# Kernel tuning notes

Hardware: AMD Instinct MI355X
Metric: run time of the kernel (lower is better)

Reference implementation:

```python
import jax, jax.numpy as jnp
import numpy as np

B, N, C, S, H, E = 4, 50000, 128, 64, 8, 800000
DH = C // H
BETA = 1.0      # frontier_beta
EPS = 1e-5      # LayerNorm eps


def setup_inputs() -> dict:
    key = jax.random.key(0)
    ks = jax.random.split(key, 12)
    sc = 1.0 / np.sqrt(C)
    x = jax.random.normal(ks[0], (B, N, C), jnp.float32)
    adj_indices = jax.random.randint(ks[1], (2, E), 0, N)
    adj_values = jax.random.uniform(ks[2], (E,), jnp.float32)
    return {
        "x": x,
        "adj_values": adj_values,
        "ln_g": jnp.ones((C,), jnp.float32),
        "ln_b": jnp.zeros((C,), jnp.float32),
        "slice_w": jax.random.normal(ks[3], (S, C), jnp.float32) * sc,
        "slice_b": jnp.zeros((S,), jnp.float32),
        "front_w": jax.random.normal(ks[4], (S, C), jnp.float32) * sc,
        "front_b": jnp.zeros((S,), jnp.float32),
        "in_w": jax.random.normal(ks[5], (3 * C, C), jnp.float32) * sc,
        "in_b": jnp.zeros((3 * C,), jnp.float32),
        "out_w": jax.random.normal(ks[6], (C, C), jnp.float32) * sc,
        "out_b": jnp.zeros((C,), jnp.float32),
        "adj_indices": adj_indices,
    }


def _layernorm(x, g, b):
    m = x.mean(-1, keepdims=True)
    v = ((x - m) ** 2).mean(-1, keepdims=True)
    return (x - m) / jnp.sqrt(v + EPS) * g + b


def reference(x, adj_values, ln_g, ln_b, slice_w, slice_b, front_w, front_b,
              in_w, in_b, out_w, out_b, adj_indices):
    h = _layernorm(x, ln_g, ln_b)                                   # (B,N,C)
    rows, cols = adj_indices[0], adj_indices[1]
    # SpMM: y[b, r] += val * h[b, c] over edges (coalesce() sums duplicates,
    # identical to segment_sum over duplicate (r,c) pairs)
    gathered = h[:, cols, :] * adj_values[None, :, None]            # (B,E,C)
    h_local = jax.vmap(
        lambda g: jax.ops.segment_sum(g, rows, num_segments=N))(gathered)
    h_frontier = h - h_local
    logits = (h @ slice_w.T + slice_b
              + BETA * (h_frontier @ front_w.T + front_b))          # (B,N,S)
    weights = jax.nn.softmax(logits, axis=-1)
    wsum = jnp.maximum(weights.sum(axis=1), 1e-8)[:, :, None]       # (B,S,1)
    slices = jnp.einsum('bns,bnc->bsc', weights, h) / wsum          # (B,S,C)
    # MultiheadAttention (batch_first, self-attention) on slice tokens
    qkv = slices @ in_w.T + in_b                                    # (B,S,3C)
    q, k, v = jnp.split(qkv, 3, axis=-1)
    split_heads = lambda t: t.reshape(B, S, H, DH).transpose(0, 2, 1, 3)
    q, k, v = split_heads(q), split_heads(k), split_heads(v)        # (B,H,S,DH)
    attn = jax.nn.softmax(
        jnp.einsum('bhqd,bhkd->bhqk', q, k) / np.sqrt(DH), axis=-1)
    o = jnp.einsum('bhqk,bhkd->bhqd', attn, v)
    o = o.transpose(0, 2, 1, 3).reshape(B, S, C)
    slices_out = o @ out_w.T + out_b                                # (B,S,C)
    out = jnp.einsum('bns,bsc->bnc', weights, slices_out)           # (B,N,C)
    return out, weights
```

## Files before the change

kernel.cpp:

```cpp
#include <hip/hip_runtime.h>
#include <math.h>

#define NB 4
#define NN 50000
#define NC 128
#define NS 64
#define NH 8
#define NE 800000
#define NDH 16
#define RTOT (NB*NN)
#define NCHUNK 128
#define NSB 196
#define LN_EPS 1e-5f

typedef __bf16 bf16;
typedef bf16 bf16x2 __attribute__((ext_vector_type(2)));
typedef bf16 bf16x4 __attribute__((ext_vector_type(4)));
typedef bf16 bf16x8 __attribute__((ext_vector_type(8)));
typedef float f32x4 __attribute__((ext_vector_type(4)));

__device__ __forceinline__ float wsum64(float v){
  #pragma unroll
  for (int off = 32; off; off >>= 1) v += __shfl_xor(v, off, 64);
  return v;
}
__device__ __forceinline__ float wmax64(float v){
  #pragma unroll
  for (int off = 32; off; off >>= 1) v = fmaxf(v, __shfl_xor(v, off, 64));
  return v;
}

__global__ void k_hist(const int* __restrict__ rows, int* __restrict__ counts){
  int e = blockIdx.x * 256 + threadIdx.x;
  if (e < NE) atomicAdd(&counts[rows[e]], 1);
}

__global__ void k_scan1(const int* __restrict__ counts,
    int* __restrict__ locpre, int* __restrict__ bsum){
  __shared__ int sh[256];
  int t = threadIdx.x;
  int gid = blockIdx.x * 256 + t;
  int v = (gid < NN) ? counts[gid] : 0;
  sh[t] = v;
  __syncthreads();
  #pragma unroll
  for (int off = 1; off < 256; off <<= 1){
    int u = (t >= off) ? sh[t - off] : 0;
    __syncthreads();
    sh[t] += u;
    __syncthreads();
  }
  if (gid < NN) locpre[gid] = sh[t] - v;
  if (t == 255) bsum[blockIdx.x] = sh[255];
}

__global__ void k_scan2(const int* __restrict__ bsum,
    int* __restrict__ bpre, int* __restrict__ offsets){
  __shared__ int sh[256];
  int t = threadIdx.x;
  int v = (t < NSB) ? bsum[t] : 0;
  sh[t] = v;
  __syncthreads();
  #pragma unroll
  for (int off = 1; off < 256; off <<= 1){
    int u = (t >= off) ? sh[t - off] : 0;
    __syncthreads();
    sh[t] += u;
    __syncthreads();
  }
  if (t < NSB) bpre[t] = sh[t] - v;
  if (t == 255) offsets[NN] = sh[255];
}

__global__ void k_scan3(const int* __restrict__ locpre, const int* __restrict__ bpre,
    int* __restrict__ offsets, int* __restrict__ offcur){
  int gid = blockIdx.x * 256 + threadIdx.x;
  if (gid < NN){
    int o = locpre[gid] + bpre[blockIdx.x];
    offsets[gid] = o;
    offcur[gid]  = o;
  }
}

__global__ void k_fill(const int* __restrict__ rows, const int* __restrict__ cols,
    const float* __restrict__ vals, int* __restrict__ offcur,
    int2* __restrict__ ev){
  int e = blockIdx.x * 256 + threadIdx.x;
  if (e < NE){
    int r = rows[e];
    int p = atomicAdd(&offcur[r], 1);
    ev[p] = make_int2(cols[e], __float_as_int(vals[e]));
  }
}

#define BM 64
#define LDP 136
__global__ __launch_bounds__(256) void k_logits(const float* __restrict__ x,
    const float* __restrict__ ln_g, const float* __restrict__ ln_be,
    const float* __restrict__ front_w, const float* __restrict__ slice_w,
    const float* __restrict__ front_b, const float* __restrict__ slice_b,
    bf16* __restrict__ h, bf16* __restrict__ hw, float* __restrict__ base){
  __shared__ bf16 hb[BM][LDP];
  __shared__ bf16 Wb[128][LDP];
  int t = threadIdx.x;
  int lane = t & 63, wv = t >> 6;
  int row0 = blockIdx.x * BM;

  for (int i = t; i < 128 * 32; i += 256){
    int r = i >> 5, c4 = (i & 31) * 4;
    const float* wsrc = (r < NS) ? (front_w + (size_t)r * NC + c4)
                                 : (slice_w + (size_t)(r - NS) * NC + c4);
    float4 v = *(const float4*)wsrc;
    bf16x4 b4 = { (bf16)v.x, (bf16)v.y, (bf16)v.z, (bf16)v.w };
    *(bf16x4*)&Wb[r][c4] = b4;
  }
  {
    float2 gg = ((const float2*)ln_g)[lane];
    float2 bb = ((const float2*)ln_be)[lane];
    const float2* x2 = (const float2*)x;
    for (int g = 0; g < 16; g += 4){
      int rl = wv * 16 + g;
      float2 v[4];
      #pragma unroll
      for (int i = 0; i < 4; ++i)
        v[i] = x2[(size_t)(row0 + rl + i) * 64 + lane];
      float s[4];
      #pragma unroll
      for (int i = 0; i < 4; ++i) s[i] = v[i].x + v[i].y;
      #pragma unroll
      for (int off = 32; off; off >>= 1)
        #pragma unroll
        for (int i = 0; i < 4; ++i) s[i] += __shfl_xor(s[i], off, 64);
      float m[4], dx[4], dy[4], q[4];
      #pragma unroll
      for (int i = 0; i < 4; ++i){
        m[i]  = s[i] * (1.0f / NC);
        dx[i] = v[i].x - m[i];
        dy[i] = v[i].y - m[i];
        q[i]  = dx[i]*dx[i] + dy[i]*dy[i];
      }
      #pragma unroll
      for (int off = 32; off; off >>= 1)
        #pragma unroll
        for (int i = 0; i < 4; ++i) q[i] += __shfl_xor(q[i], off, 64);
      #pragma unroll
      for (int i = 0; i < 4; ++i){
        float var = q[i] * (1.0f / NC);
        float rs  = rsqrtf(var + LN_EPS);
        bf16x2 o2 = { (bf16)(dx[i] * rs * gg.x + bb.x),
                      (bf16)(dy[i] * rs * gg.y + bb.y) };
        *(bf16x2*)&hb[rl + i][lane * 2] = o2;
        *(bf16x2*)&h[(size_t)(row0 + rl + i) * NC + lane * 2] = o2;
      }
    }
  }
  __syncthreads();

  int kg = lane >> 4;
  int lr = lane & 15;
  f32x4 acc[8];
  #pragma unroll
  for (int nt = 0; nt < 8; ++nt) acc[nt] = (f32x4){0.f,0.f,0.f,0.f};

  #pragma unroll
  for (int ks = 0; ks < 4; ++ks){
    bf16x8 af = *(bf16x8*)&hb[wv*16 + lr][ks*32 + kg*8];
    #pragma unroll
    for (int nt = 0; nt < 8; ++nt){
      bf16x8 bw = *(bf16x8*)&Wb[nt*16 + lr][ks*32 + kg*8];
      acc[nt] = __builtin_amdgcn_mfma_f32_16x16x32_bf16(af, bw, acc[nt], 0, 0, 0);
    }
  }

  float bias[4];
  #pragma unroll
  for (int nt = 0; nt < 4; ++nt)
    bias[nt] = front_b[nt*16 + lr] + slice_b[nt*16 + lr];

  #pragma unroll
  for (int q = 0; q < 4; ++q){
    int rl = wv*16 + kg*4 + q;
    size_t gr = (size_t)(row0 + rl);
    #pragma unroll
    for (int nt = 0; nt < 4; ++nt){
      float f = acc[nt][q], sl = acc[nt+4][q];
      hw[gr * NS + nt*16 + lr]   = (bf16)f;
      base[gr * NS + nt*16 + lr] = f + sl + bias[nt];
    }
  }
}

__global__ __launch_bounds__(256) void k_smax(const bf16* __restrict__ hw,
    const int* __restrict__ offsets, const int2* __restrict__ ev,
    float* __restrict__ wbuf){
  int t = threadIdx.x;
  int lane = t & 63, wv = t >> 6;
  int n = blockIdx.x * 4 + wv;
  int j0 = offsets[n], j1 = offsets[n + 1];

  const bf16* h0 = hw + lane;
  const bf16* h1 = h0 + (size_t)NN * NS;
  const bf16* h2 = h1 + (size_t)NN * NS;
  const bf16* h3 = h2 + (size_t)NN * NS;

  float a0 = wbuf[(size_t)(0*NN + n) * NS + lane];
  float a1 = wbuf[(size_t)(1*NN + n) * NS + lane];
  float a2 = wbuf[(size_t)(2*NN + n) * NS + lane];
  float a3 = wbuf[(size_t)(3*NN + n) * NS + lane];

  for (int jb = j0; jb < j1; jb += 64){
    int cnt = j1 - jb; if (cnt > 64) cnt = 64;
    int jj = jb + lane;
    int2 e = ev[jj < j1 ? jj : j0];
    int u = 0;
    #define EDGE(U) {                                                   \
      int   c  = __builtin_amdgcn_readlane(e.x, (U));                   \
      float vv = __int_as_float(__builtin_amdgcn_readlane(e.y, (U)));   \
      size_t o = (size_t)c << 6;                                        \
      float t0 = (float)h0[o], t1 = (float)h1[o];                       \
      float t2 = (float)h2[o], t3 = (float)h3[o];                       \
      a0 = fmaf(-vv, t0, a0); a1 = fmaf(-vv, t1, a1);                   \
      a2 = fmaf(-vv, t2, a2); a3 = fmaf(-vv, t3, a3); }
    for (; u + 4 <= cnt; u += 4){
      EDGE(u) EDGE(u+1) EDGE(u+2) EDGE(u+3)
    }
    for (; u < cnt; ++u){ EDGE(u) }
    #undef EDGE
  }

  float m0=a0, m1=a1, m2=a2, m3=a3;
  #pragma unroll
  for (int off = 32; off; off >>= 1){
    m0 = fmaxf(m0, __shfl_xor(m0, off, 64));
    m1 = fmaxf(m1, __shfl_xor(m1, off, 64));
    m2 = fmaxf(m2, __shfl_xor(m2, off, 64));
    m3 = fmaxf(m3, __shfl_xor(m3, off, 64));
  }
  float e0 = __expf(a0 - m0), e1 = __expf(a1 - m1);
  float e2 = __expf(a2 - m2), e3 = __expf(a3 - m3);
  float s0=e0, s1=e1, s2=e2, s3=e3;
  #pragma unroll
  for (int off = 32; off; off >>= 1){
    s0 += __shfl_xor(s0, off, 64);
    s1 += __shfl_xor(s1, off, 64);
    s2 += __shfl_xor(s2, off, 64);
    s3 += __shfl_xor(s3, off, 64);
  }
  wbuf[(size_t)(0*NN + n) * NS + lane] = e0 / s0;
  wbuf[(size_t)(1*NN + n) * NS + lane] = e1 / s1;
  wbuf[(size_t)(2*NN + n) * NS + lane] = e2 / s2;
  wbuf[(size_t)(3*NN + n) * NS + lane] = e3 / s3;
}

__global__ __launch_bounds__(256) void k_slices(const float* __restrict__ wbuf,
    const bf16* __restrict__ h, float* __restrict__ partial,
    float* __restrict__ wspart){
  __shared__ float wst[8][NS];
  __shared__ float hst[8][NC];
  int b = blockIdx.y, chunk = blockIdx.x;
  const int per = (NN + NCHUNK - 1) / NCHUNK;
  int nbeg = chunk * per, nend = min(NN, nbeg + per);
  int t = threadIdx.x;
  int s0 = (t >> 5) * 8, c0 = (t & 31) * 4;
  float acc[8][4];
  #pragma unroll
  for (int i = 0; i < 8; ++i)
    #pragma unroll
    for (int j = 0; j < 4; ++j) acc[i][j] = 0.f;
  float wsacc = 0.f;
  const float* wb = wbuf + (size_t)b * NN * NS;
  const bf16*  hb = h    + (size_t)b * NN * NC;
  for (int nb = nbeg; nb < nend; nb += 8){
    int cnt = min(8, nend - nb);
    for (int i = t; i < 8 * NS; i += 256){
      int rr = i >> 6;
      wst[rr][i & 63] = (rr < cnt) ? wb[(size_t)(nb + rr)*NS + (i & 63)] : 0.f;
    }
    {
      int rr = t >> 5, cc = (t & 31) * 4;
      if (rr < cnt){
        bf16x4 v = *(const bf16x4*)&hb[(size_t)(nb + rr)*NC + cc];
        hst[rr][cc+0] = (float)v[0]; hst[rr][cc+1] = (float)v[1];
        hst[rr][cc+2] = (float)v[2]; hst[rr][cc+3] = (float)v[3];
      } else {
        hst[rr][cc+0] = 0.f; hst[rr][cc+1] = 0.f;
        hst[rr][cc+2] = 0.f; hst[rr][cc+3] = 0.f;
      }
    }
    __syncthreads();
    #pragma unroll
    for (int rr = 0; rr < 8; ++rr){
      float4 hv = *(const float4*)&hst[rr][c0];
      #pragma unroll
      for (int i = 0; i < 8; ++i){
        float wv = wst[rr][s0 + i];
        acc[i][0] = fmaf(wv, hv.x, acc[i][0]);
        acc[i][1] = fmaf(wv, hv.y, acc[i][1]);
        acc[i][2] = fmaf(wv, hv.z, acc[i][2]);
        acc[i][3] = fmaf(wv, hv.w, acc[i][3]);
      }
    }
    if (t < NS){
      #pragma unroll
      for (int rr = 0; rr < 8; ++rr) wsacc += wst[rr][t];
    }
    __syncthreads();
  }
  float* dst = partial + (size_t)(b * NCHUNK + chunk) * NS * NC;
  #pragma unroll
  for (int i = 0; i < 8; ++i)
    *(float4*)&dst[(s0 + i)*NC + c0] =
        make_float4(acc[i][0], acc[i][1], acc[i][2], acc[i][3]);
  if (t < NS) wspart[(size_t)(b * NCHUNK + chunk) * NS + t] = wsacc;
}

__global__ void k_wsum(const float* __restrict__ wspart, float* __restrict__ wsumg){
  int t = threadIdx.x;
  int b = t >> 6, s = t & 63;
  float a = 0.f;
  for (int ch = 0; ch < NCHUNK; ++ch)
    a += wspart[(size_t)(b * NCHUNK + ch) * NS + s];
  wsumg[t] = fmaxf(a, 1e-8f);
}

__global__ void k_redslices(const float* __restrict__ partial,
    const float* __restrict__ wsumg, float* __restrict__ slices){
  int idx = blockIdx.x * 256 + threadIdx.x;
  if (idx >= NB * NS * NC) return;
  int b  = idx / (NS * NC);
  int sc = idx - b * NS * NC;
  int s  = sc >> 7;
  const float* p = partial + (size_t)b * NCHUNK * NS * NC + sc;
  float acc = 0.f;
  for (int ch = 0; ch < NCHUNK; ++ch) acc += p[(size_t)ch * NS * NC];
  slices[idx] = acc / wsumg[b * NS + s];
}

__global__ __launch_bounds__(256) void k_mha(const float* __restrict__ slices,
    const float* __restrict__ in_w, const float* __restrict__ in_b,
    float* __restrict__ obuf){
  __shared__ float sl[NS][NC];
  __shared__ float qs[NS][NDH], ks[NS][NDH], vs[NS][NDH];
  __shared__ float att[NS][NS];
  int b  = blockIdx.x >> 3;
  int hh = blockIdx.x & 7;
  int t  = threadIdx.x;
  const float* slb = slices + (size_t)b * NS * NC;
  for (int i = t; i < NS * NC; i += 256) ((float*)sl)[i] = slb[i];
  __syncthreads();
  for (int p = t; p < NS * NDH; p += 256){
    int s = p >> 4, d = p & 15;
    int rq = hh * NDH + d;
    const float* wq = in_w + (size_t)rq * NC;
    const float* wk = in_w + (size_t)(NC + rq) * NC;
    const float* wv = in_w + (size_t)(2*NC + rq) * NC;
    float aq = 0.f, ak = 0.f, av = 0.f;
    for (int c = 0; c < NC; ++c){
      float hv = sl[s][c];
      aq = fmaf(hv, wq[c], aq); ak = fmaf(hv, wk[c], ak); av = fmaf(hv, wv[c], av);
    }
    qs[s][d] = aq + in_b[rq];
    ks[s][d] = ak + in_b[NC + rq];
    vs[s][d] = av + in_b[2*NC + rq];
  }
  __syncthreads();
  for (int p = t; p < NS * NS; p += 256){
    int si = p >> 6, sj = p & 63;
    float a = 0.f;
    #pragma unroll
    for (int d = 0; d < NDH; ++d) a = fmaf(qs[si][d], ks[sj][d], a);
    att[si][sj] = a * 0.25f;
  }
  __syncthreads();
  int lane = t & 63, wv_ = t >> 6;
  for (int si = wv_; si < NS; si += 4){
    float a  = att[si][lane];
    float m  = wmax64(a);
    float e  = __expf(a - m);
    float sm = wsum64(e);
    att[si][lane] = e / sm;
  }
  __syncthreads();
  for (int p = t; p < NS * NDH; p += 256){
    int s = p >> 4, d = p & 15;
    float a = 0.f;
    #pragma unroll 8
    for (int j = 0; j < NS; ++j) a = fmaf(att[s][j], vs[j][d], a);
    obuf[((size_t)(b*NS + s))*NC + hh*NDH + d] = a;
  }
}

__global__ void k_outproj(const float* __restrict__ obuf,
    const float* __restrict__ out_w, const float* __restrict__ out_b,
    float* __restrict__ so){
  int idx = blockIdx.x * 256 + threadIdx.x;
  if (idx >= NB * NS * NC) return;
  int c  = idx & 127;
  int bs = idx >> 7;
  const float* orow = obuf  + (size_t)bs * NC;
  const float* wrow = out_w + (size_t)c  * NC;
  float a = 0.f;
  #pragma unroll 8
  for (int j = 0; j < NC; ++j) a = fmaf(orow[j], wrow[j], a);
  so[idx] = a + out_b[c];
}

__global__ __launch_bounds__(256) void k_final(const float* __restrict__ wbuf,
    const float* __restrict__ so, float* __restrict__ out){
  __shared__ float sl[NS][NC];
  __shared__ float wt[4][4][NS];
  int b = blockIdx.y;
  for (int i = threadIdx.x; i < NS * NC; i += 256)
    ((float*)sl)[i] = so[(size_t)b * NS * NC + i];
  __syncthreads();
  int lane = threadIdx.x & 63, wv = threadIdx.x >> 6;
  const float* wb = wbuf + (size_t)b * NN * NS;
  float* ob = out + (size_t)b * NN * NC;
  int step = gridDim.x * 16;
  for (int n0 = (blockIdx.x * 4 + wv) * 4; n0 < NN; n0 += step){
    #pragma unroll
    for (int r = 0; r < 4; ++r)
      wt[wv][r][lane] = wb[(size_t)(n0 + r)*NS + lane];
    float2 a0 = {0,0}, a1 = {0,0}, a2 = {0,0}, a3 = {0,0};
    #pragma unroll 8
    for (int s = 0; s < NS; ++s){
      float2 sv = *(const float2*)&sl[s][lane * 2];
      float w0 = wt[wv][0][s], w1 = wt[wv][1][s], w2 = wt[wv][2][s], w3 = wt[wv][3][s];
      a0.x = fmaf(w0, sv.x, a0.x); a0.y = fmaf(w0, sv.y, a0.y);
      a1.x = fmaf(w1, sv.x, a1.x); a1.y = fmaf(w1, sv.y, a1.y);
      a2.x = fmaf(w2, sv.x, a2.x); a2.y = fmaf(w2, sv.y, a2.y);
      a3.x = fmaf(w3, sv.x, a3.x); a3.y = fmaf(w3, sv.y, a3.y);
    }
    *(float2*)&ob[(size_t)(n0+0)*NC + lane*2] = a0;
    *(float2*)&ob[(size_t)(n0+1)*NC + lane*2] = a1;
    *(float2*)&ob[(size_t)(n0+2)*NC + lane*2] = a2;
    *(float2*)&ob[(size_t)(n0+3)*NC + lane*2] = a3;
  }
}

extern "C" void kernel_launch(void* const* d_in, const int* in_sizes, int n_in,
                              void* d_out, int out_size, void* d_ws, size_t ws_size,
                              hipStream_t stream){
  const float* x          = (const float*)d_in[0];
  const float* adj_values = (const float*)d_in[1];
  const float* ln_g       = (const float*)d_in[2];
  const float* ln_b       = (const float*)d_in[3];
  const float* slice_w    = (const float*)d_in[4];
  const float* slice_b    = (const float*)d_in[5];
  const float* front_w    = (const float*)d_in[6];
  const float* front_b    = (const float*)d_in[7];
  const float* in_w       = (const float*)d_in[8];
  const float* in_b       = (const float*)d_in[9];
  const float* out_w      = (const float*)d_in[10];
  const float* out_b      = (const float*)d_in[11];
  const int*   adj        = (const int*)d_in[12];
  const int*   rows = adj;
  const int*   cols = adj + NE;

  float* outp = (float*)d_out;
  float* wbuf = outp + (size_t)NB * NN * NC;

  char* wsb = (char*)d_ws;
  size_t off = 0;
  auto alloc = [&](size_t bytes) -> void* {
    void* p = wsb + off;
    off += (bytes + 255) & ~(size_t)255;
    return p;
  };
  bf16*  hw     = (bf16*) alloc((size_t)NB*NN*NS*2);
  bf16*  h16    = (bf16*) alloc((size_t)NB*NN*NC*2);
  int2*  ev     = (int2*) alloc((size_t)NE*8);
  int*   counts = (int*)  alloc((size_t)NN*4);
  int*   offsets= (int*)  alloc((size_t)(NN+1)*4);
  int*   offcur = (int*)  alloc((size_t)NN*4);
  int*   locpre = (int*)  alloc((size_t)NN*4);
  int*   bsum   = (int*)  alloc((size_t)NSB*4);
  int*   bpre   = (int*)  alloc((size_t)NSB*4);
  float* wsumg  = (float*)alloc((size_t)NB*NS*4);
  float* wspart = (float*)alloc((size_t)NB*NCHUNK*NS*4);
  float* obuf   = (float*)alloc((size_t)NB*NS*NC*4);
  float* so     = (float*)alloc((size_t)NB*NS*NC*4);
  float* slices = (float*)alloc((size_t)NB*NS*NC*4);
  float* partial = (float*)hw;

  hipMemsetAsync(counts, 0, (size_t)NN*4, stream);

  k_hist   <<<(NE+255)/256, 256, 0, stream>>>(rows, counts);
  k_scan1  <<<NSB, 256, 0, stream>>>(counts, locpre, bsum);
  k_scan2  <<<1, 256, 0, stream>>>(bsum, bpre, offsets);
  k_scan3  <<<NSB, 256, 0, stream>>>(locpre, bpre, offsets, offcur);
  k_fill   <<<(NE+255)/256, 256, 0, stream>>>(rows, cols, adj_values, offcur, ev);
  k_logits <<<RTOT/BM, 256, 0, stream>>>(x, ln_g, ln_b, front_w, slice_w, front_b, slice_b, h16, hw, wbuf);
  k_smax   <<<NN/4, 256, 0, stream>>>(hw, offsets, ev, wbuf);
  k_slices <<<dim3(NCHUNK, NB), 256, 0, stream>>>(wbuf, h16, partial, wspart);
  k_wsum   <<<1, 256, 0, stream>>>(wspart, wsumg);
  k_redslices<<<(NB*NS*NC+255)/256, 256, 0, stream>>>(partial, wsumg, slices);
  k_mha    <<<NB*NH, 256, 0, stream>>>(slices, in_w, in_b, obuf);
  k_outproj<<<(NB*NS*NC+255)/256, 256, 0, stream>>>(obuf, out_w, out_b, so);
  k_final  <<<dim3(512, NB), 256, 0, stream>>>(wbuf, so, outp);
}
```

Before: 462.7 us.

## Restructure slice accumulation to read h directly and widen row batches

The slice-reduction kernel now stages 32 rows of softmax weights in shared memory per iteration instead of 8, and reads bf16 h directly from global memory with 8-wide vector loads rather than converting it through shared memory. The per-thread tile changes from 8x4 to 4x8. This cuts barrier count and shared-memory traffic. The chunk count rises to 192 for more blocks, which means a larger partial buffer to reduce afterwards. The LayerNorm prologue also batches 8 rows per wave iteration instead of 4 to expose more memory-level parallelism.

```diff
diff --git a/kernel.cpp b/kernel.cpp
--- a/kernel.cpp
+++ b/kernel.cpp
@@ -9,7 +9,7 @@
 #define NE 800000
 #define NDH 16
 #define RTOT (NB*NN)
-#define NCHUNK 128
+#define NCHUNK 192
 #define NSB 196
 #define LN_EPS 1e-5f
 
@@ -118,33 +118,33 @@
     float2 gg = ((const float2*)ln_g)[lane];
     float2 bb = ((const float2*)ln_be)[lane];
     const float2* x2 = (const float2*)x;
-    for (int g = 0; g < 16; g += 4){
+    for (int g = 0; g < 16; g += 8){
       int rl = wv * 16 + g;
-      float2 v[4];
-      #pragma unroll
-      for (int i = 0; i < 4; ++i)
+      float2 v[8];
+      #pragma unroll
+      for (int i = 0; i < 8; ++i)
         v[i] = x2[(size_t)(row0 + rl + i) * 64 + lane];
-      float s[4];
-      #pragma unroll
-      for (int i = 0; i < 4; ++i) s[i] = v[i].x + v[i].y;
+      float s[8];
+      #pragma unroll
+      for (int i = 0; i < 8; ++i) s[i] = v[i].x + v[i].y;
       #pragma unroll
       for (int off = 32; off; off >>= 1)
         #pragma unroll
-        for (int i = 0; i < 4; ++i) s[i] += __shfl_xor(s[i], off, 64);
-      float m[4], dx[4], dy[4], q[4];
-      #pragma unroll
-      for (int i = 0; i < 4; ++i){
-        m[i]  = s[i] * (1.0f / NC);
-        dx[i] = v[i].x - m[i];
-        dy[i] = v[i].y - m[i];
+        for (int i = 0; i < 8; ++i) s[i] += __shfl_xor(s[i], off, 64);
+      float dx[8], dy[8], q[8];
+      #pragma unroll
+      for (int i = 0; i < 8; ++i){
+        float m = s[i] * (1.0f / NC);
+        dx[i] = v[i].x - m;
+        dy[i] = v[i].y - m;
         q[i]  = dx[i]*dx[i] + dy[i]*dy[i];
       }
       #pragma unroll
       for (int off = 32; off; off >>= 1)
         #pragma unroll
-        for (int i = 0; i < 4; ++i) q[i] += __shfl_xor(q[i], off, 64);
-      #pragma unroll
-      for (int i = 0; i < 4; ++i){
+        for (int i = 0; i < 8; ++i) q[i] += __shfl_xor(q[i], off, 64);
+      #pragma unroll
+      for (int i = 0; i < 8; ++i){
         float var = q[i] * (1.0f / NC);
         float rs  = rsqrtf(var + LN_EPS);
         bf16x2 o2 = { (bf16)(dx[i] * rs * gg.x + bb.x),
@@ -255,62 +255,57 @@
 __global__ __launch_bounds__(256) void k_slices(const float* __restrict__ wbuf,
     const bf16* __restrict__ h, float* __restrict__ partial,
     float* __restrict__ wspart){
-  __shared__ float wst[8][NS];
-  __shared__ float hst[8][NC];
+  __shared__ float wst[32][NS];
   int b = blockIdx.y, chunk = blockIdx.x;
   const int per = (NN + NCHUNK - 1) / NCHUNK;
   int nbeg = chunk * per, nend = min(NN, nbeg + per);
   int t = threadIdx.x;
-  int s0 = (t >> 5) * 8, c0 = (t & 31) * 4;
-  float acc[8][4];
-  #pragma unroll
-  for (int i = 0; i < 8; ++i)
+  int sg = (t >> 4) * 4;
+  int cg = (t & 15) * 8;
+  float acc[4][8];
+  #pragma unroll
+  for (int i = 0; i < 4; ++i)
     #pragma unroll
-    for (int j = 0; j < 4; ++j) acc[i][j] = 0.f;
+    for (int j = 0; j < 8; ++j) acc[i][j] = 0.f;
   float wsacc = 0.f;
   const float* wb = wbuf + (size_t)b * NN * NS;
   const bf16*  hb = h    + (size_t)b * NN * NC;
-  for (int nb = nbeg; nb < nend; nb += 8){
-    int cnt = min(8, nend - nb);
-    for (int i = t; i < 8 * NS; i += 256){
-      int rr = i >> 6;
-      wst[rr][i & 63] = (rr < cnt) ? wb[(size_t)(nb + rr)*NS + (i & 63)] : 0.f;
-    }
-    {
-      int rr = t >> 5, cc = (t & 31) * 4;
-      if (rr < cnt){
-        bf16x4 v = *(const bf16x4*)&hb[(size_t)(nb + rr)*NC + cc];
-        hst[rr][cc+0] = (float)v[0]; hst[rr][cc+1] = (float)v[1];
-        hst[rr][cc+2] = (float)v[2]; hst[rr][cc+3] = (float)v[3];
-      } else {
-        hst[rr][cc+0] = 0.f; hst[rr][cc+1] = 0.f;
-        hst[rr][cc+2] = 0.f; hst[rr][cc+3] = 0.f;
-      }
-    }
-    __syncthreads();
-    #pragma unroll
-    for (int rr = 0; rr < 8; ++rr){
-      float4 hv = *(const float4*)&hst[rr][c0];
-      #pragma unroll
-      for (int i = 0; i < 8; ++i){
-        float wv = wst[rr][s0 + i];
-        acc[i][0] = fmaf(wv, hv.x, acc[i][0]);
-        acc[i][1] = fmaf(wv, hv.y, acc[i][1]);
-        acc[i][2] = fmaf(wv, hv.z, acc[i][2]);
-        acc[i][3] = fmaf(wv, hv.w, acc[i][3]);
-      }
+  for (int nb = nbeg; nb < nend; nb += 32){
+    int cnt = min(32, nend - nb);
+    for (int i = t; i < 32 * 32; i += 256){
+      int rr = i >> 5, cc = (i & 31) * 2;
+      float2 v = (rr < cnt) ? *(const float2*)&wb[(size_t)(nb + rr)*NS + cc]
+                            : make_float2(0.f, 0.f);
+      *(float2*)&wst[rr][cc] = v;
+    }
+    __syncthreads();
+    #pragma unroll 4
+    for (int r = 0; r < cnt; ++r){
+      bf16x8 hv8 = *(const bf16x8*)&hb[(size_t)(nb + r)*NC + cg];
+      float hv[8];
+      #pragma unroll
+      for (int j = 0; j < 8; ++j) hv[j] = (float)hv8[j];
+      float4 wv = *(const float4*)&wst[r][sg];
+      float wv4[4] = { wv.x, wv.y, wv.z, wv.w };
+      #pragma unroll
+      for (int i = 0; i < 4; ++i)
+        #pragma unroll
+        for (int j = 0; j < 8; ++j)
+          acc[i][j] = fmaf(wv4[i], hv[j], acc[i][j]);
     }
     if (t < NS){
-      #pragma unroll
-      for (int rr = 0; rr < 8; ++rr) wsacc += wst[rr][t];
+      for (int r = 0; r < cnt; ++r) wsacc += wst[r][t];
     }
     __syncthreads();
   }
   float* dst = partial + (size_t)(b * NCHUNK + chunk) * NS * NC;
   #pragma unroll
-  for (int i = 0; i < 8; ++i)
-    *(float4*)&dst[(s0 + i)*NC + c0] =
+  for (int i = 0; i < 4; ++i){
+    *(float4*)&dst[(sg + i)*NC + cg]     =
         make_float4(acc[i][0], acc[i][1], acc[i][2], acc[i][3]);
+    *(float4*)&dst[(sg + i)*NC + cg + 4] =
+        make_float4(acc[i][4], acc[i][5], acc[i][6], acc[i][7]);
+  }
   if (t < NS) wspart[(size_t)(b * NCHUNK + chunk) * NS + t] = wsacc;
 }
 
```

Measured after the change: 444.1 us. 1.04x faster.
